# Optimization experiments

Hardware: AMD Instinct MI355X
Metric: run time of the kernel (lower is better)

Reference implementation:

```python
import jax, jax.numpy as jnp
import numpy as np

CH, K, RR = 12, 7, 4  # pooled temporal size / involution kernel / reduction ratio

def conv3d(x, w, pad):
    return jax.lax.conv_general_dilated(x, w, (1, 1, 1), [(pad, pad)] * 3,
                                        dimension_numbers=('NCDHW', 'OIDHW', 'NCDHW'))

def conv1x1(x, w, b=None):
    out = jnp.einsum('oi,bidhw->bodhw', w, x)
    return out if b is None else out + b[None, :, None, None, None]

def adaptive_pool(x, outs):
    b, c, D, H, W = x.shape
    fd, fh, fw = D // outs[0], H // outs[1], W // outs[2]
    return x.reshape(b, c, outs[0], fd, outs[1], fh, outs[2], fw).mean(axis=(3, 5, 7))

def bnorm(x, g, b):
    m = x.mean(axis=(0, 2, 3, 4), keepdims=True)
    v = x.var(axis=(0, 2, 3, 4), keepdims=True)
    return (x - m) * jax.lax.rsqrt(v + 1e-5) * g[None, :, None, None, None] + b[None, :, None, None, None]

def setup_inputs():
    key = jax.random.key(0)
    ks = jax.random.split(key, 12)
    c = 64; cr = c // RR; Cf = c + CH * cr; M = CH * K * K
    def nrm(k_, shape, fan_in):
        return jax.random.normal(k_, shape, jnp.float32) / np.sqrt(fan_in)
    return {
        'x_CT': jax.random.normal(ks[0], (2, c, 8, 56, 56), jnp.float32),
        'x_WSI': jax.random.normal(ks[1], (2, c, 12, 56, 56), jnp.float32),
        'W_ct': nrm(ks[2], (c, c), c), 'b_ct': jnp.zeros((c,), jnp.float32),
        'W_wsi': nrm(ks[3], (c, c), c), 'b_wsi': jnp.zeros((c,), jnp.float32),
        'W_att': nrm(ks[4], (1 + CH, M, 5, 5, 5), M * 125),
        'W_inv': nrm(ks[5], (K * K, M), M), 'b_inv': jnp.zeros((K * K,), jnp.float32),
        'W_rr': nrm(ks[6], (cr, c, 3, 3, 3), c * 27),
        'g1': jnp.ones((Cf,), jnp.float32), 'be1': jnp.zeros((Cf,), jnp.float32),
        'g2': jnp.ones((Cf,), jnp.float32), 'be2': jnp.zeros((Cf,), jnp.float32),
        'W_p1': nrm(ks[7], (Cf, Cf), Cf), 'b_p1': jnp.zeros((Cf,), jnp.float32),
        'W_p2': nrm(ks[8], (c, Cf), Cf), 'b_p2': jnp.zeros((c,), jnp.float32),
    }

def reference(x_CT, x_WSI, W_ct, b_ct, W_wsi, b_wsi, W_att, W_inv, b_inv, W_rr,
              g1, be1, g2, be2, W_p1, b_p1, W_p2, b_p2):
    b, c, t, h, w = x_CT.shape
    cr = c // RR
    M = CH * K * K
    x1 = conv1x1(x_CT, W_ct, b_ct)
    xw1 = adaptive_pool(conv1x1(x_WSI, W_wsi, b_wsi), (CH, K, K))       # (b,c,CH,K,K)
    # cross-modal bmm: (b, thw, c) x (b, c, M) -> (b, thw, M)
    multi = jnp.einsum('bnc,bcm->bnm', x1.reshape(b, c, t * h * w).transpose(0, 2, 1),
                       xw1.reshape(b, c, M))
    feature = multi.reshape(b, t, h, w, M).transpose(0, 4, 1, 2, 3)     # (b,M,t,h,w)
    Att = jax.nn.sigmoid(conv3d(feature, W_att, 2))                      # (b,1+CH,t,h,w)
    xw3 = conv3d(x_WSI, W_rr, 1)                                         # (b,cr,CH,h,w)
    xw5 = jnp.broadcast_to(xw3.reshape(b, cr * CH, 1, h, w), (b, cr * CH, t, h, w))
    x_FS = jnp.concatenate([x_CT, xw5], axis=1)                          # (b,Cf,t,h,w)
    Att_CT = jnp.broadcast_to(Att[:, :1], (b, c, t, h, w))
    Att_WSI = jnp.tile(Att[:, 1:].reshape(b, CH, t, h * w), (1, 1, cr, 1)).reshape(b, CH * cr, t, h, w)
    Att_FS = jnp.concatenate([Att_CT, Att_WSI], axis=1)
    x_Att = x_FS * Att_FS + x_FS
    # per-pixel dynamic kernel: (b,t,K,K,h,w)
    kern = conv1x1(feature, W_inv, b_inv).transpose(0, 2, 1, 3, 4).reshape(b, t, K, K, h, w)
    x_Att1 = jax.nn.relu(bnorm(conv1x1(x_Att, W_p1, b_p1), g1, be1))
    pad = K // 2
    xp = jnp.pad(x_Att1, ((0, 0), (0, 0), (0, 0), (pad, pad), (pad, pad)))
    out = jnp.zeros_like(x_Att1)
    for i in range(K):                                                   # fixed 7x7 involution taps
        for j in range(K):
            out = out + kern[:, None, :, i, j] * xp[:, :, :, i:i + h, j:j + w]
    return conv1x1(bnorm(out, g2, be2) + x_Att, W_p2, b_p2)
```

## Files before the change

### kernel.cpp

```cpp
#include <hip/hip_runtime.h>
#include <hip/hip_bf16.h>
#include <math.h>

typedef __hip_bfloat16 bf16;
typedef unsigned short us;
typedef __attribute__((ext_vector_type(8))) short short8v;
typedef __attribute__((ext_vector_type(4))) float f32x4;
#define DEV static __device__ __forceinline__
DEV float b2f(bf16 x){ return __bfloat162float(x); }
DEV bf16  f2b(float x){ return __float2bfloat16(x); }
DEV us    f2u(float x){ bf16 h=f2b(x); return *(us*)&h; }
DEV float u2f(us u){ return __uint_as_float(((unsigned)u)<<16); }
DEV float blo(unsigned int w){ return __uint_as_float(w<<16); }
DEV float bhi(unsigned int w){ return __uint_as_float(w&0xffff0000u); }
DEV float ldin(const void* p, long i, int f){
  return f ? ((const float*)p)[i] : b2f(((const bf16*)p)[i]);
}

#define PP 25088

#define POOLo  3211264L
#define XW1o   3286528L
#define WXo    3361792L
#define WXTo   3569792L
#define WIXo   3825792L
#define ATTo   3832064L
#define KERNo  4484352L
#define XW3o   6942976L
#define STATo  8147200L
#define FLAGo  8149248L
#define WFo    8149264L
#define WATTFo 8267280L
#define WINVFo 9222784L
#define BF16o  9251600L
#define WRR2o  WXo
#define bX1T   3211264L
#define bXATT  8028160L
#define bY1    20873216L
#define bINV   33718272L
#define bWP1B  46563328L
#define bWP2B  46628864L
#define bW2S   46645248L
#define bXWT   bY1
#define oWCT   0
#define oBCT   4096
#define oWWSI  4160
#define oBWSI  8256
#define oWRR   8320
#define oBINV  35968
#define oWP1   36032
#define oWP2   101568
#define oBP2   117952

__global__ void k_detect(const us* raw, int* flag){
  int t = threadIdx.x;
  us u = raw[2*t];
  int e = (u>>7)&0xFF;
  int hit = (e >= 137);
  unsigned long long m = __ballot(hit);
  if(t==0) flag[0] = (__popcll(m) >= 8) ? 1 : 0;
}

__global__ void k_prep(const void* Watt,const void* Winv,const void* Wct,const void* bct,
                       const void* Wwsi,const void* bwsi,const void* Wrr,const void* binv,
                       const void* Wp1,const void* Wp2,const void* bp2,
                       float* Wattf,float* Winvf,float* wf,us* Wp1b,us* Wp2b,const int* flag){
  int i = blockIdx.x*256 + threadIdx.x;
  int f = flag[0];
  if(i<955500) Wattf[i]=ldin(Watt,i,f);
  if(i<28812)  Winvf[i]=ldin(Winv,i,f);
  if(i<65536)  Wp1b[i]=f2u(ldin(Wp1,i,f));
  else if(i<81920) Wp2b[i-65536]=f2u(ldin(Wp2,i-65536,f));
  if (i < 4096){ int co=i>>6, ci=i&63; wf[oWCT + ci*64+co] = ldin(Wct,i,f); }
  else if (i < 4160){ wf[i] = ldin(bct,i-4096,f); }
  else if (i < 8256){ wf[i] = ldin(Wwsi,i-4160,f); }
  else if (i < 8320){ wf[i] = ldin(bwsi,i-8256,f); }
  else if (i < 35968){ int l=i-8320; int co=l/1728, r=l%1728, ci=r/27, tp=r%27;
                       wf[oWRR + (ci*27+tp)*16+co] = ldin(Wrr,l,f); }
  else if (i < 36017){ wf[oBINV + (i-35968)] = ldin(binv,i-35968,f); }
  else if (i < 36032){ }
  else if (i < 118016){
    int l=i-36032;
    if(l<65536){ int co=l>>8, ci=l&255; wf[oWP1 + ci*256+co] = ldin(Wp1,l,f); }
    else if(l<81920){ int l2=l-65536; int o=l2>>8, ci=l2&255; wf[oWP2 + ci*64+o] = ldin(Wp2,l2,f); }
    else if(l<81984){ wf[oBP2 + (l-81920)] = ldin(bp2,l-81920,f); }
  }
}

__global__ void k_wsit(const void* xwsi_r, const int* flag, us* xwt){
  __shared__ us tl[64*68];
  int tid=threadIdx.x; int p0=blockIdx.x*64; int d=blockIdx.y; int b=blockIdx.z;
  int f=flag[0];
  #pragma unroll
  for(int k=0;k<16;k++){
    int idx=k*256+tid; int px=idx&63, c=idx>>6;
    float v = ldin(xwsi_r, ((long)(b*64+c)*12+d)*3136 + p0+px, f);
    tl[px*68+c] = f2u(v);
  }
  __syncthreads();
  #pragma unroll
  for(int k=0;k<16;k++){
    int idx=k*256+tid; int px=idx>>6, ch=idx&63;
    xwt[((size_t)(b*12+d)*3136 + p0+px)*64 + ch] = tl[px*68+ch];
  }
}

__global__ __launch_bounds__(64) void k_poolxw1(const us* xwt, const float* wf, float* xw1){
  __shared__ float pl[64];
  int c=threadIdx.x; int m=blockIdx.x; int b=blockIdx.y;
  int d=m/49, r=m%49, ii=r/7, jj=r%7;
  const us* src = xwt + ((size_t)(b*12+d)*3136 + (ii*8)*56 + jj*8)*64 + c;
  float s=0;
  #pragma unroll
  for(int u=0;u<8;u++)
    #pragma unroll
    for(int v=0;v<8;v++) s += u2f(src[(size_t)(u*56+v)*64]);
  pl[c] = s*(1.f/64.f);
  __syncthreads();
  const float* w = wf + oWWSI + c*64;
  float o = wf[oBWSI + c];
  for(int ci=0;ci<64;ci++) o += w[ci]*pl[ci];
  xw1[(b*588+m)*64+c] = o;
}

__global__ void k_Wx(const float* Wattf, const float* xw1, float* Wx){
  int i = blockIdx.x*256+threadIdx.x; if(i>=208000) return;
  int c=i&63; int r=i>>6; int tap=r%125; int o=(r/125)%13; int b=r/1625;
  const float* wa = Wattf + (size_t)o*588*125 + tap;
  const float* xp = xw1 + b*588*64 + c;
  float s=0;
  for(int m=0;m<588;m++) s += wa[(size_t)m*125] * xp[m*64];
  Wx[i]=s;
}

__global__ void k_Wfrag(const float* Wx, us* Wf){
  int i = blockIdx.x*256+threadIdx.x; if(i>=256000) return;
  int j=i&7; int m=(i>>3)&15; int kg=(i>>7)&3; int ch=(i>>9)&1;
  int r=i>>10; int tap=r%125; int b=r/125;
  int c = ch*32 + kg*8 + j;
  float v = (m<13) ? Wx[((size_t)(b*13+m)*125+tap)*64 + c] : 0.f;
  Wf[i] = f2u(v);
}

__global__ void k_rrfrag(const float* wf, us* Wrr2){
  int i = blockIdx.x*256+threadIdx.x; if(i>=27648) return;
  int j=i&7; int l=(i>>3)&63; int kg=(i>>9)&1; int td=i>>10;
  int m=l&15, g=l>>4;
  int c = kg*32 + g*8 + j;
  Wrr2[i] = f2u(wf[oWRR + (c*27+td)*16 + m]);
}

__global__ void k_Winvx(const float* Winvf, const float* xw1, float* Wix){
  int i = blockIdx.x*256+threadIdx.x; if(i>=6272) return;
  int ms = blockIdx.y;
  int kk=i%49; int c=(i/49)&63; int b=i/3136;
  int m0=ms*74; int m1=m0+74; if(m1>588) m1=588;
  const float* xp = xw1 + b*588*64 + c;
  float s=0;
  for(int m=m0;m<m1;m++) s += Winvf[kk*588+m] * xp[m*64];
  atomicAdd(&Wix[i], s);
}

__global__ void k_x1(const void* xct_r, const int* flag, const float* wf, us* x1t){
  int p = blockIdx.x*256+threadIdx.x;
  int co0 = blockIdx.y*16; int b = blockIdx.z;
  float acc[16];
  #pragma unroll
  for(int o=0;o<16;o++) acc[o]=wf[oBCT+co0+o];
  int f=flag[0];
  if(f){
    const float* xp = (const float*)xct_r + (size_t)b*64*PP + p;
    for(int ci=0;ci<64;ci++){
      float xv = xp[(size_t)ci*PP];
      const float* w = wf + oWCT + ci*64 + co0;
      #pragma unroll
      for(int o=0;o<16;o++) acc[o] += w[o]*xv;
    }
  } else {
    const bf16* xp = (const bf16*)xct_r + (size_t)b*64*PP + p;
    for(int ci=0;ci<64;ci++){
      float xv = b2f(xp[(size_t)ci*PP]);
      const float* w = wf + oWCT + ci*64 + co0;
      #pragma unroll
      for(int o=0;o<16;o++) acc[o] += w[o]*xv;
    }
  }
  unsigned int pk[8];
  #pragma unroll
  for(int o2=0;o2<8;o2++)
    pk[o2] = (unsigned)f2u(acc[2*o2]) | ((unsigned)f2u(acc[2*o2+1])<<16);
  us* xo = x1t + ((size_t)(b*PP)+p)*64 + co0;
  *(uint4*)xo     = make_uint4(pk[0],pk[1],pk[2],pk[3]);
  *(uint4*)(xo+8) = make_uint4(pk[4],pk[5],pk[6],pk[7]);
}

__global__ __launch_bounds__(256) void k_att(const us* x1t, const us* Wf, float* att){
  __shared__ short xt[10368];
  int tid=threadIdx.x;
  int tile=blockIdx.x, t=blockIdx.y, b=blockIdx.z;
  int y0=(tile/7)*8, x0=(tile%7)*8;
  int w=tid>>6, l=tid&63;
  int pc=l&7, pr=(l>>3)&1, g=l>>4;
  f32x4 acc0={0,0,0,0}, acc1={0,0,0,0};
  int bbase = ((2*w+pr)*12 + pc)*72 + g*8;
  const us* Wb = Wf + (size_t)b*128000 + l*8;
  for(int dt=0;dt<5;dt++){
    int ti=t+dt-2;
    if(ti<0||ti>=8) continue;
    __syncthreads();
    for(int e=tid;e<1152;e+=256){
      int px=e>>3, q=e&7;
      int row=px/12, col=px-row*12;
      int gy=y0+row-2, gx=x0+col-2;
      uint4 v={0,0,0,0};
      if((unsigned)gy<56u && (unsigned)gx<56u)
        v = *(const uint4*)(x1t + ((size_t)(b*PP) + ti*3136 + gy*56 + gx)*64 + q*8);
      *(uint4*)&xt[px*72 + q*8] = v;
    }
    __syncthreads();
    const us* Wd = Wb + dt*25600;
    #pragma unroll
    for(int dy=0;dy<5;dy++){
      #pragma unroll
      for(int dx=0;dx<5;dx++){
        int off = bbase + dy*864 + dx*72;
        short8v a0 = *(const short8v*)(Wd + (dy*5+dx)*1024);
        short8v b0 = *(const short8v*)&xt[off];
        acc0 = __builtin_amdgcn_mfma_f32_16x16x32_bf16(a0,b0,acc0,0,0,0);
        short8v a1 = *(const short8v*)(Wd + (dy*5+dx)*1024 + 512);
        short8v b1 = *(const short8v*)&xt[off+32];
        acc1 = __builtin_amdgcn_mfma_f32_16x16x32_bf16(a1,b1,acc1,0,0,0);
      }
    }
  }
  int px=l&15; int epc=px&7, epr=px>>3;
  size_t pbase=(size_t)t*3136+(size_t)(y0+2*w+epr)*56+x0+epc;
  #pragma unroll
  for(int r=0;r<4;r++){
    int o=g*4+r;
    if(o<13){
      float s=acc0[r]+acc1[r];
      att[((size_t)b*13+o)*PP+pbase]=1.f/(1.f+__expf(-s));
    }
  }
}

__global__ void k_kern(const us* x1t, const float* Wix, const float* wf, float* kern){
  int p = blockIdx.x*256+threadIdx.x; int b=blockIdx.y;
  float acc[49];
  #pragma unroll
  for(int kk=0;kk<49;kk++) acc[kk]=wf[oBINV+kk];
  const us* xp = x1t + ((size_t)b*PP + p)*64;
  #pragma unroll
  for(int c8=0;c8<8;c8++){
    uint4 v = *(const uint4*)(xp + c8*8);
    const us* vp=(const us*)&v;
    #pragma unroll
    for(int j=0;j<8;j++){
      float xv = u2f(vp[j]);
      const float* w = Wix + (b*64+c8*8+j)*49;
      #pragma unroll
      for(int kk=0;kk<49;kk++) acc[kk]+=w[kk]*xv;
    }
  }
  float* out = kern + (size_t)b*49*PP + p;
  #pragma unroll
  for(int kk=0;kk<49;kk++) out[(size_t)kk*PP]=acc[kk];
}

__global__ __launch_bounds__(256) void k_rr(const us* xwt, const us* Wrr2, bf16* xw3){
  __shared__ short xt[7200];
  int tid=threadIdx.x;
  int tile=blockIdx.x, d=blockIdx.y, b=blockIdx.z;
  int y0=(tile/7)*8, x0=(tile%7)*8;
  int w=tid>>6, l=tid&63;
  int pc=l&7, pr=(l>>3)&1, g=l>>4;
  f32x4 acc0={0,0,0,0}, acc1={0,0,0,0};
  int bbase = ((2*w+pr)*10 + pc)*72 + g*8;
  const us* Wl = Wrr2 + l*8;
  for(int dz=0;dz<3;dz++){
    int di=d+dz-1;
    if(di<0||di>=12) continue;
    __syncthreads();
    for(int e=tid;e<800;e+=256){
      int px=e>>3, q=e&7;
      int row=px/10, col=px-row*10;
      int gy=y0+row-1, gx=x0+col-1;
      uint4 v={0,0,0,0};
      if((unsigned)gy<56u && (unsigned)gx<56u)
        v = *(const uint4*)(xwt + ((size_t)(b*12+di)*3136 + gy*56 + gx)*64 + q*8);
      *(uint4*)&xt[px*72 + q*8] = v;
    }
    __syncthreads();
    const us* Wd = Wl + dz*9216;
    #pragma unroll
    for(int tap=0;tap<9;tap++){
      int dy=tap/3, dx=tap-dy*3;
      int off = bbase + (dy*10+dx)*72;
      short8v a0 = *(const short8v*)(Wd + tap*1024);
      short8v b0 = *(const short8v*)&xt[off];
      acc0 = __builtin_amdgcn_mfma_f32_16x16x32_bf16(a0,b0,acc0,0,0,0);
      short8v a1 = *(const short8v*)(Wd + tap*1024 + 512);
      short8v b1 = *(const short8v*)&xt[off+32];
      acc1 = __builtin_amdgcn_mfma_f32_16x16x32_bf16(a1,b1,acc1,0,0,0);
    }
  }
  int px=l&15; int epc=px&7, epr=px>>3;
  size_t pp=(size_t)(y0+2*w+epr)*56 + x0+epc;
  #pragma unroll
  for(int r=0;r<4;r++){
    int o=g*4+r;
    xw3[((size_t)(b*16+o)*12+d)*3136 + pp] = f2b(acc0[r]+acc1[r]);
  }
}

__global__ void k_xatt(const void* xct_r, const int* flag, const bf16* xw3,
                       const float* att, us* xattT){
  __shared__ us tl[64*258];
  int tid=threadIdx.x; int p0=blockIdx.x*64; int b=blockIdx.y;
  int f=flag[0];
  for(int k=0;k<64;k++){
    int idx=k*256+tid; int ch=idx>>6, pp=idx&63;
    int p=p0+pp;
    float v;
    if(ch<64){
      long ix = (long)(b*64+ch)*PP+p;
      float xv;
      if(f) xv = ((const float*)xct_r)[ix]; else xv = b2f(((const bf16*)xct_r)[ix]);
      v = xv * (1.f+att[(size_t)b*13*PP+p]);
    } else {
      int q=ch-64; int co=q/12, dd=q-co*12;
      int s=p%3136;
      v = b2f(xw3[((size_t)(b*16+co)*12+dd)*3136+s]) * (1.f+att[((size_t)b*13+1+q/16)*PP+p]);
    }
    tl[pp*258+ch]=f2u(v);
  }
  __syncthreads();
  for(int k=0;k<64;k++)
    xattT[((size_t)b*PP + p0+k)*256 + tid] = tl[k*258+tid];
}

__global__ __launch_bounds__(256) void k_p1(const us* xattT, const us* Wp1b, us* y1T){
  __shared__ us wt[16384];
  int tid=threadIdx.x; int w=tid>>6, l=tid&63;
  int pt=blockIdx.x, qtr=blockIdx.y, b=blockIdx.z;
  int co0 = qtr*64;
  #pragma unroll
  for(int it=0;it<8;it++){
    int f = it*256+tid;
    int n=f>>9, kc=(f>>6)&7, lane=f&63;
    int co = co0 + n*16 + (lane&15);
    int ci = (lane>>4)*8 + kc*32;
    uint4 v = *(const uint4*)(Wp1b + (size_t)co*256 + ci);
    *(uint4*)(wt + f*8) = v;
  }
  __syncthreads();
  int p0 = pt*64 + w*16;
  const us* xa = xattT + ((size_t)b*PP + p0 + (l&15))*256 + ((l>>4)*8);
  f32x4 acc[4];
  #pragma unroll
  for(int n=0;n<4;n++) acc[n]=(f32x4){0,0,0,0};
  for(int kc=0;kc<8;kc++){
    short8v a = *(const short8v*)(xa + kc*32);
    #pragma unroll
    for(int n=0;n<4;n++){
      short8v bf = *(const short8v*)(wt + ((n*8+kc)*64 + l)*8);
      acc[n] = __builtin_amdgcn_mfma_f32_16x16x32_bf16(a,bf,acc[n],0,0,0);
    }
  }
  int col=l&15, rowb=(l>>4)*4;
  us* yo = y1T + ((size_t)b*PP + p0)*256 + co0;
  #pragma unroll
  for(int n=0;n<4;n++)
    #pragma unroll
    for(int r=0;r<4;r++)
      yo[(size_t)(rowb+r)*256 + n*16 + col] = f2u(acc[n][r]);
}

__global__ void k_stats(const us* src, float* sum, float* sq){
  int tid=threadIdx.x; int pt=blockIdx.x, b=blockIdx.y;
  const us* p = src + ((size_t)b*PP + pt*64)*256 + tid;
  float s=0,q=0;
  #pragma unroll 8
  for(int i=0;i<64;i++){ float v=u2f(p[(size_t)i*256]); s+=v; q+=v*v; }
  atomicAdd(&sum[tid],s); atomicAdd(&sq[tid],q);
}
__global__ void k_finstat(const float* sum, const float* sq, const void* g, const void* be,
                          const int* flag, float* sc, float* sh){
  int ch=threadIdx.x;
  int f=flag[0];
  float m = sum[ch]*(1.f/50176.f);
  float v = sq[ch]*(1.f/50176.f) - m*m;
  float s = ldin(g,ch,f) * rsqrtf(v+1e-5f);
  sc[ch]=s; sh[ch]=ldin(be,ch,f) - m*s;
}

__global__ __launch_bounds__(256) void k_inv(const us* y1T, const float* sc1, const float* sh1,
                                             const float* kern, us* invT){
  __shared__ __align__(16) us xt[196*72];
  int tid=threadIdx.x;
  int bx=blockIdx.x, by=blockIdx.y, bz=blockIdx.z;
  int t=bz&7, b=bz>>3;
  int y0=(bx/7)*8, x0=(bx%7)*8, c0=by*64;
  int w=tid>>6, l=tid&63;
  int ty=l>>3, tx=l&7;
  int segb = c0 + (tid&7)*8;
  float scr[8], shr[8];
  #pragma unroll
  for(int j=0;j<8;j++){ scr[j]=sc1[segb+j]; shr[j]=sh1[segb+j]; }
  for(int e=tid;e<1568;e+=256){
    int row=e>>3, seg=e&7;
    int yy=row/14, xx=row%14;
    int gy=y0+yy-3, gx=x0+xx-3;
    uint4 o4={0,0,0,0};
    if(gy>=0&&gy<56&&gx>=0&&gx<56){
      uint4 v = *(const uint4*)&y1T[((size_t)b*PP + t*3136 + gy*56+gx)*256 + c0 + seg*8];
      const us* vp=(const us*)&v;
      us r[8];
      #pragma unroll
      for(int j=0;j<8;j++){
        float x = u2f(vp[j]);
        x = x*scr[j]+shr[j]; x = x>0.f?x:0.f;
        r[j]=f2u(x);
      }
      o4 = *(const uint4*)r;
    }
    *(uint4*)&xt[row*72+seg*8]=o4;
  }
  float kr[49];
  size_t pxs=(size_t)t*3136 + (y0+ty)*56 + x0+tx;
  #pragma unroll
  for(int kk=0;kk<49;kk++) kr[kk]=kern[((size_t)b*49+kk)*PP+pxs];
  __syncthreads();
  #pragma unroll
  for(int s=0;s<2;s++){
    int sub=2*w+s;
    float acc[8];
    #pragma unroll
    for(int e=0;e<8;e++) acc[e]=0;
    for(int i=0;i<7;i++){
      #pragma unroll
      for(int j=0;j<7;j++){
        uint4 u = *(const uint4*)&xt[((ty+i)*14+tx+j)*72 + sub*8];
        float kv = kr[i*7+j];
        acc[0]+=kv*blo(u.x); acc[1]+=kv*bhi(u.x);
        acc[2]+=kv*blo(u.y); acc[3]+=kv*bhi(u.y);
        acc[4]+=kv*blo(u.z); acc[5]+=kv*bhi(u.z);
        acc[6]+=kv*blo(u.w); acc[7]+=kv*bhi(u.w);
      }
    }
    unsigned pk[4];
    #pragma unroll
    for(int e=0;e<4;e++)
      pk[e] = (unsigned)f2u(acc[2*e]) | ((unsigned)f2u(acc[2*e+1])<<16);
    *(uint4*)&invT[((size_t)b*PP+pxs)*256 + c0 + sub*8] = make_uint4(pk[0],pk[1],pk[2],pk[3]);
  }
}

__global__ void k_w2s(const float* wf, const float* sc2, const float* sh2,
                      us* W2sb, float* bias2){
  __shared__ float red[256];
  int o=blockIdx.x, ci=threadIdx.x;
  float wv = wf[oWP2 + ci*64 + o];
  W2sb[o*256+ci] = f2u(wv * sc2[ci]);
  red[ci] = wv * sh2[ci];
  __syncthreads();
  for(int st=128;st>0;st>>=1){ if(ci<st) red[ci]+=red[ci+st]; __syncthreads(); }
  if(ci==0) bias2[o] = wf[oBP2+o] + red[0];
}

__global__ __launch_bounds__(256) void k_final(const us* invT, const us* xattT,
                                               const us* W2sb, const us* Wp2b,
                                               const float* bias2, float* out){
  __shared__ us wt[32768];
  int tid=threadIdx.x; int w=tid>>6, l=tid&63;
  int pt=blockIdx.x, b=blockIdx.y;
  #pragma unroll
  for(int it=0;it<16;it++){
    int f = it*256+tid;
    int which = f>>11;
    int g = f&2047;
    int n=g>>9, kc=(g>>6)&7, lane=g&63;
    int co = n*16 + (lane&15);
    int ci = (lane>>4)*8 + kc*32;
    const us* src = which ? Wp2b : W2sb;
    uint4 v = *(const uint4*)(src + (size_t)co*256 + ci);
    *(uint4*)(wt + f*8) = v;
  }
  __syncthreads();
  int p0 = pt*64 + w*16;
  size_t abase = ((size_t)b*PP + p0 + (l&15))*256 + ((l>>4)*8);
  f32x4 acc[4];
  #pragma unroll
  for(int n=0;n<4;n++) acc[n]=(f32x4){0,0,0,0};
  for(int kc=0;kc<8;kc++){
    short8v ai = *(const short8v*)(invT + abase + kc*32);
    short8v ax = *(const short8v*)(xattT + abase + kc*32);
    #pragma unroll
    for(int n=0;n<4;n++){
      short8v b1 = *(const short8v*)(wt + ((n*8+kc)*64 + l)*8);
      acc[n] = __builtin_amdgcn_mfma_f32_16x16x32_bf16(ai,b1,acc[n],0,0,0);
      short8v b2 = *(const short8v*)(wt + 16384 + ((n*8+kc)*64 + l)*8);
      acc[n] = __builtin_amdgcn_mfma_f32_16x16x32_bf16(ax,b2,acc[n],0,0,0);
    }
  }
  int col=l&15, rowb=(l>>4)*4;
  #pragma unroll
  for(int n=0;n<4;n++){
    float bb = bias2[n*16+col];
    #pragma unroll
    for(int r=0;r<4;r++)
      out[((size_t)b*64 + n*16+col)*PP + p0 + rowb + r] = acc[n][r] + bb;
  }
}

extern "C" void kernel_launch(void* const* d_in, const int* in_sizes, int n_in,
                              void* d_out, int out_size, void* d_ws, size_t ws_size,
                              hipStream_t stream){
  const void* xct_r =d_in[0];
  const void* xwsi_r=d_in[1];
  const void* Wct =d_in[2];
  const void* bct =d_in[3];
  const void* Wwsi=d_in[4];
  const void* bwsi=d_in[5];
  const void* Watt=d_in[6];
  const void* Winv=d_in[7];
  const void* binv=d_in[8];
  const void* Wrr =d_in[9];
  const void* g1  =d_in[10];
  const void* be1 =d_in[11];
  const void* g2  =d_in[12];
  const void* be2 =d_in[13];
  const void* Wp1 =d_in[14];
  const void* Wp2 =d_in[16];
  const void* bp2 =d_in[17];
  float* ws=(float*)d_ws;
  float* xw1=ws+XW1o;
  float* Wx=ws+WXo; float* Wix=ws+WIXo;
  float* att=ws+ATTo; float* kern=ws+KERNo;
  us* Wf=(us*)(ws+WXTo);
  us* Wrr2=(us*)(ws+WRR2o);
  bf16* xw3=(bf16*)(ws+XW3o);
  float* stat=ws+STATo; float* wf=ws+WFo;
  float* Wattf=ws+WATTFo; float* Winvf=ws+WINVFo;
  float* bias2=ws+WATTFo;
  int* flag=(int*)(ws+FLAGo);
  bf16* bfb=(bf16*)(ws+BF16o);
  us* x1t=(us*)(bfb+bX1T);
  us* xattT=(us*)(bfb+bXATT); us* y1T=(us*)(bfb+bY1); us* invT=(us*)(bfb+bINV);
  us* Wp1b=(us*)(bfb+bWP1B); us* Wp2b=(us*)(bfb+bWP2B); us* W2sb=(us*)(bfb+bW2S);
  us* xwt=(us*)(bfb+bXWT);
  float* sum1=stat; float* sq1=stat+256; float* sum2=stat+512; float* sq2=stat+768;
  float* sc1=stat+1024; float* sh1=stat+1280; float* sc2=stat+1536; float* sh2=stat+1792;

  hipMemsetAsync(stat,0,4096,stream);
  hipMemsetAsync(Wix,0,6272*4,stream);
  k_detect<<<1,64,0,stream>>>((const us*)xct_r,flag);
  k_prep  <<<3733,256,0,stream>>>(Watt,Winv,Wct,bct,Wwsi,bwsi,Wrr,binv,Wp1,Wp2,bp2,
                                  Wattf,Winvf,wf,Wp1b,Wp2b,flag);
  k_wsit  <<<dim3(49,12,2),256,0,stream>>>(xwsi_r,flag,xwt);
  k_poolxw1<<<dim3(588,2),64,0,stream>>>(xwt,wf,xw1);
  k_Wx    <<<813,256,0,stream>>>(Wattf,xw1,Wx);
  k_Wfrag <<<1000,256,0,stream>>>(Wx,Wf);
  k_rrfrag<<<108,256,0,stream>>>(wf,Wrr2);
  k_Winvx <<<dim3(25,8),256,0,stream>>>(Winvf,xw1,Wix);
  k_x1    <<<dim3(98,4,2),256,0,stream>>>(xct_r,flag,wf,x1t);
  k_att   <<<dim3(49,8,2),256,0,stream>>>(x1t,Wf,att);
  k_kern  <<<dim3(98,2),256,0,stream>>>(x1t,Wix,wf,kern);
  k_rr    <<<dim3(49,12,2),256,0,stream>>>(xwt,Wrr2,xw3);
  k_xatt  <<<dim3(392,2),256,0,stream>>>(xct_r,flag,xw3,att,xattT);
  k_p1    <<<dim3(392,4,2),256,0,stream>>>(xattT,Wp1b,y1T);
  k_stats <<<dim3(392,2),256,0,stream>>>(y1T,sum1,sq1);
  k_finstat<<<1,256,0,stream>>>(sum1,sq1,g1,be1,flag,sc1,sh1);
  k_inv   <<<dim3(49,4,16),256,0,stream>>>(y1T,sc1,sh1,kern,invT);
  k_stats <<<dim3(392,2),256,0,stream>>>(invT,sum2,sq2);
  k_finstat<<<1,256,0,stream>>>(sum2,sq2,g2,be2,flag,sc2,sh2);
  k_w2s   <<<64,256,0,stream>>>(wf,sc2,sh2,W2sb,bias2);
  k_final <<<dim3(392,2),256,0,stream>>>(invT,xattT,W2sb,Wp2b,bias2,(float*)d_out);
}
```

Before: 370.9 us.

## Fuse batchnorm statistics into p1 and involution kernels; store dynamic kernel as bf16

```diff
diff --git a/kernel.cpp b/kernel.cpp
--- a/kernel.cpp
+++ b/kernel.cpp
@@ -245,7 +245,7 @@
   }
 }
 
-__global__ void k_kern(const us* x1t, const float* Wix, const float* wf, float* kern){
+__global__ void k_kern(const us* x1t, const float* Wix, const float* wf, bf16* kern){
   int p = blockIdx.x*256+threadIdx.x; int b=blockIdx.y;
   float acc[49];
   #pragma unroll
@@ -263,9 +263,9 @@
       for(int kk=0;kk<49;kk++) acc[kk]+=w[kk]*xv;
     }
   }
-  float* out = kern + (size_t)b*49*PP + p;
-  #pragma unroll
-  for(int kk=0;kk<49;kk++) out[(size_t)kk*PP]=acc[kk];
+  bf16* out = kern + (size_t)b*49*PP + p;
+  #pragma unroll
+  for(int kk=0;kk<49;kk++) out[(size_t)kk*PP]=f2b(acc[kk]);
 }
 
 __global__ __launch_bounds__(256) void k_rr(const us* xwt, const us* Wrr2, bf16* xw3){
@@ -340,7 +340,8 @@
     xattT[((size_t)b*PP + p0+k)*256 + tid] = tl[k*258+tid];
 }
 
-__global__ __launch_bounds__(256) void k_p1(const us* xattT, const us* Wp1b, us* y1T){
+__global__ __launch_bounds__(256) void k_p1(const us* xattT, const us* Wp1b, us* y1T,
+                                            float* sum1, float* sq1){
   __shared__ us wt[16384];
   int tid=threadIdx.x; int w=tid>>6, l=tid&63;
   int pt=blockIdx.x, qtr=blockIdx.y, b=blockIdx.z;
@@ -371,20 +372,23 @@
   int col=l&15, rowb=(l>>4)*4;
   us* yo = y1T + ((size_t)b*PP + p0)*256 + co0;
   #pragma unroll
-  for(int n=0;n<4;n++)
-    #pragma unroll
-    for(int r=0;r<4;r++)
-      yo[(size_t)(rowb+r)*256 + n*16 + col] = f2u(acc[n][r]);
-}
-
-__global__ void k_stats(const us* src, float* sum, float* sq){
-  int tid=threadIdx.x; int pt=blockIdx.x, b=blockIdx.y;
-  const us* p = src + ((size_t)b*PP + pt*64)*256 + tid;
-  float s=0,q=0;
-  #pragma unroll 8
-  for(int i=0;i<64;i++){ float v=u2f(p[(size_t)i*256]); s+=v; q+=v*v; }
-  atomicAdd(&sum[tid],s); atomicAdd(&sq[tid],q);
-}
+  for(int n=0;n<4;n++){
+    float sv=0, qv=0;
+    #pragma unroll
+    for(int r=0;r<4;r++){
+      float x = acc[n][r];
+      yo[(size_t)(rowb+r)*256 + n*16 + col] = f2u(x);
+      sv += x; qv += x*x;
+    }
+    sv += __shfl_xor(sv,16,64); sv += __shfl_xor(sv,32,64);
+    qv += __shfl_xor(qv,16,64); qv += __shfl_xor(qv,32,64);
+    if((l>>4)==0){
+      atomicAdd(&sum1[co0+n*16+col],sv);
+      atomicAdd(&sq1[co0+n*16+col],qv);
+    }
+  }
+}
+
 __global__ void k_finstat(const float* sum, const float* sq, const void* g, const void* be,
                           const int* flag, float* sc, float* sh){
   int ch=threadIdx.x;
@@ -396,7 +400,8 @@
 }
 
 __global__ __launch_bounds__(256) void k_inv(const us* y1T, const float* sc1, const float* sh1,
-                                             const float* kern, us* invT){
+                                             const bf16* kern, us* invT,
+                                             float* sum2, float* sq2){
   __shared__ __align__(16) us xt[196*72];
   int tid=threadIdx.x;
   int bx=blockIdx.x, by=blockIdx.y, bz=blockIdx.z;
@@ -430,7 +435,7 @@
   float kr[49];
   size_t pxs=(size_t)t*3136 + (y0+ty)*56 + x0+tx;
   #pragma unroll
-  for(int kk=0;kk<49;kk++) kr[kk]=kern[((size_t)b*49+kk)*PP+pxs];
+  for(int kk=0;kk<49;kk++) kr[kk]=b2f(kern[((size_t)b*49+kk)*PP+pxs]);
   __syncthreads();
   #pragma unroll
   for(int s=0;s<2;s++){
@@ -454,6 +459,16 @@
     for(int e=0;e<4;e++)
       pk[e] = (unsigned)f2u(acc[2*e]) | ((unsigned)f2u(acc[2*e+1])<<16);
     *(uint4*)&invT[((size_t)b*PP+pxs)*256 + c0 + sub*8] = make_uint4(pk[0],pk[1],pk[2],pk[3]);
+    #pragma unroll
+    for(int e=0;e<8;e++){
+      float sv=acc[e], qv=acc[e]*acc[e];
+      #pragma unroll
+      for(int m=32;m>0;m>>=1){ sv+=__shfl_xor(sv,m,64); qv+=__shfl_xor(qv,m,64); }
+      if(l==0){
+        atomicAdd(&sum2[c0+sub*8+e],sv);
+        atomicAdd(&sq2[c0+sub*8+e],qv);
+      }
+    }
   }
 }
 
@@ -537,7 +552,8 @@
   float* ws=(float*)d_ws;
   float* xw1=ws+XW1o;
   float* Wx=ws+WXo; float* Wix=ws+WIXo;
-  float* att=ws+ATTo; float* kern=ws+KERNo;
+  float* att=ws+ATTo;
+  bf16* kern=(bf16*)(ws+KERNo);
   us* Wf=(us*)(ws+WXTo);
   us* Wrr2=(us*)(ws+WRR2o);
   bf16* xw3=(bf16*)(ws+XW3o);
@@ -569,11 +585,9 @@
   k_kern  <<<dim3(98,2),256,0,stream>>>(x1t,Wix,wf,kern);
   k_rr    <<<dim3(49,12,2),256,0,stream>>>(xwt,Wrr2,xw3);
   k_xatt  <<<dim3(392,2),256,0,stream>>>(xct_r,flag,xw3,att,xattT);
-  k_p1    <<<dim3(392,4,2),256,0,stream>>>(xattT,Wp1b,y1T);
-  k_stats <<<dim3(392,2),256,0,stream>>>(y1T,sum1,sq1);
+  k_p1    <<<dim3(392,4,2),256,0,stream>>>(xattT,Wp1b,y1T,sum1,sq1);
   k_finstat<<<1,256,0,stream>>>(sum1,sq1,g1,be1,flag,sc1,sh1);
-  k_inv   <<<dim3(49,4,16),256,0,stream>>>(y1T,sc1,sh1,kern,invT);
-  k_stats <<<dim3(392,2),256,0,stream>>>(invT,sum2,sq2);
+  k_inv   <<<dim3(49,4,16),256,0,stream>>>(y1T,sc1,sh1,kern,invT,sum2,sq2);
   k_finstat<<<1,256,0,stream>>>(sum2,sq2,g2,be2,flag,sc2,sh2);
   k_w2s   <<<64,256,0,stream>>>(wf,sc2,sh2,W2sb,bias2);
   k_final <<<dim3(392,2),256,0,stream>>>(invT,xattT,W2sb,Wp2b,bias2,(float*)d_out);
```

Result: slower. 695.5 us (+87.5%).
